# Kernel tuning notes

Hardware: AMD Instinct MI355X
Metric: run time of the kernel (lower is better)

## Reference

```python
import jax, jax.numpy as jnp
import numpy as np

B, H, E = 1024, 2048, 1024

def _xavier(key, shape):
    # torch xavier_normal_ on [1, out, in]: std = sqrt(2/(fan_in+fan_out)) over last two dims
    fan_out, fan_in = shape[-2], shape[-1]
    std = (2.0 / (fan_in + fan_out)) ** 0.5
    return jax.random.normal(key, shape, jnp.float32) * std

def setup_inputs() -> dict:
    key = jax.random.key(0)
    ks = jax.random.split(key, 17)
    inp = {
        'x': jax.random.normal(ks[0], (B, E, 1), jnp.float32),
        'c': jax.random.normal(ks[1], (B, H, 1), jnp.float32),
        'h': jax.random.normal(ks[2], (B, H, 1), jnp.float32),
        'W_xi': _xavier(ks[3], (1, H, E)), 'W_hi': _xavier(ks[4], (1, H, H)), 'B_i': _xavier(ks[5], (1, H, 1)),
        'W_xg': _xavier(ks[6], (1, H, E)), 'W_hg': _xavier(ks[7], (1, H, H)), 'B_g': _xavier(ks[8], (1, H, 1)),
        'W_xf': _xavier(ks[9], (1, H, E)), 'W_hf': _xavier(ks[10], (1, H, H)), 'B_f': _xavier(ks[11], (1, H, 1)),
        'W_xo': _xavier(ks[12], (1, H, E)), 'W_ho': _xavier(ks[13], (1, H, H)), 'B_o': _xavier(ks[14], (1, H, 1)),
        'W_hy': _xavier(ks[15], (1, E, H)), 'B_y': _xavier(ks[16], (1, E, 1)),
    }
    return inp

def reference(x, c, h, W_xi, W_hi, B_i, W_xg, W_hg, B_g, W_xf, W_hf, B_f, W_xo, W_ho, B_o, W_hy, B_y):
    # jnp.matmul broadcasts the leading batch dim: [1,H,E] @ [B,E,1] -> [B,H,1]
    i = jax.nn.sigmoid(jnp.matmul(W_xi, x) + jnp.matmul(W_hi, h) + B_i)
    g = jnp.tanh(jnp.matmul(W_xg, x) + jnp.matmul(W_hg, h) + B_g)
    f = jax.nn.sigmoid(jnp.matmul(W_xf, x) + jnp.matmul(W_hf, h) + B_f)
    c_new = f * c + i * g
    o = jax.nn.sigmoid(jnp.matmul(W_xo, x) + jnp.matmul(W_ho, h) + B_o)
    h_new = o * c_new  # NOTE: source uses o*c (no tanh), faithful to original
    y = jnp.tanh(jnp.matmul(W_hy, h_new) + B_y)
    return (y, c_new, h_new)
```

## Files before the change

kernel.cpp:

```cpp
#include <hip/hip_runtime.h>

#define B_SZ 1024
#define H_SZ 2048
#define E_SZ 1024

typedef float  f32x4 __attribute__((ext_vector_type(4)));
typedef short  s16x8 __attribute__((ext_vector_type(8)));

__device__ __forceinline__ unsigned short f2bf(float f) {
    unsigned u = __float_as_uint(f);
    u = u + 0x7fffu + ((u >> 16) & 1u);
    return (unsigned short)(u >> 16);
}
__device__ __forceinline__ float bf2f(unsigned short s) {
    return __uint_as_float(((unsigned)s) << 16);
}

struct CastArgs {
    const float*    src[11];
    unsigned short* dst[11];
    int             n[11];
};

__global__ __launch_bounds__(256) void cast_kernel(CastArgs a) {
    const int arr = blockIdx.y;
    const int n = a.n[arr];
    const float* __restrict__ s = a.src[arr];
    unsigned short* __restrict__ d = a.dst[arr];
    const int stride = gridDim.x * 256 * 4;
    for (int i = (blockIdx.x * 256 + threadIdx.x) * 4; i < n; i += stride) {
        float4 v = *(const float4*)(s + i);
        ushort4 o;
        o.x = f2bf(v.x); o.y = f2bf(v.y); o.z = f2bf(v.z); o.w = f2bf(v.w);
        *(ushort4*)(d + i) = o;
    }
}

__device__ __forceinline__ void gemm_accum(
    const unsigned short* __restrict__ A,
    const unsigned short* __restrict__ W,
    int ld, int kLen, int m0, int n0,
    unsigned short* lA, unsigned short* lB,
    f32x4 acc[4][4], int t)
{
    const int lane = t & 63;
    const int w    = t >> 6;
    const int wr   = (w >> 1) << 6;
    const int wc   = (w & 1) << 6;
    const int lr   = lane & 15;
    const int kq   = (lane >> 4) << 3;

    const int r0   = t >> 2;
    const int col0 = (t & 3) << 3;

    for (int k0 = 0; k0 < kLen; k0 += 32) {
        const unsigned short* ga0 = A + (size_t)(m0 + r0) * ld + (k0 + col0);
        const unsigned short* ga1 = ga0 + (size_t)64 * ld;
        const unsigned short* gb0 = W + (size_t)(n0 + r0) * ld + (k0 + col0);
        const unsigned short* gb1 = gb0 + (size_t)64 * ld;
        __builtin_amdgcn_global_load_lds(
            (const __attribute__((address_space(1))) unsigned int*)ga0,
            (__attribute__((address_space(3))) unsigned int*)(lA + t * 8), 16, 0, 0);
        __builtin_amdgcn_global_load_lds(
            (const __attribute__((address_space(1))) unsigned int*)ga1,
            (__attribute__((address_space(3))) unsigned int*)(lA + (t + 256) * 8), 16, 0, 0);
        __builtin_amdgcn_global_load_lds(
            (const __attribute__((address_space(1))) unsigned int*)gb0,
            (__attribute__((address_space(3))) unsigned int*)(lB + t * 8), 16, 0, 0);
        __builtin_amdgcn_global_load_lds(
            (const __attribute__((address_space(1))) unsigned int*)gb1,
            (__attribute__((address_space(3))) unsigned int*)(lB + (t + 256) * 8), 16, 0, 0);
        __syncthreads();

        s16x8 af[4], bfr[4];
#pragma unroll
        for (int i = 0; i < 4; ++i)
            af[i] = *(const s16x8*)(lA + (wr + i * 16 + lr) * 32 + kq);
#pragma unroll
        for (int j = 0; j < 4; ++j)
            bfr[j] = *(const s16x8*)(lB + (wc + j * 16 + lr) * 32 + kq);
#pragma unroll
        for (int i = 0; i < 4; ++i)
#pragma unroll
            for (int j = 0; j < 4; ++j)
                acc[i][j] = __builtin_amdgcn_mfma_f32_16x16x32_bf16(
                    af[i], bfr[j], acc[i][j], 0, 0, 0);
        __syncthreads();
    }
}

__global__ __launch_bounds__(256) void gates_kernel(
    const unsigned short* __restrict__ Xb,
    const unsigned short* __restrict__ Hb,
    const unsigned short* __restrict__ Wxb,
    const unsigned short* __restrict__ Whb,
    const float* __restrict__ bi, const float* __restrict__ bg,
    const float* __restrict__ bff, const float* __restrict__ bo,
    unsigned short* __restrict__ Z)
{
    __shared__ unsigned short lA[128 * 32];
    __shared__ unsigned short lB[128 * 32];
    const int t   = threadIdx.x;
    const int b   = blockIdx.x;
    const int xcd = b & 7;
    const int i_  = b >> 3;
    const int nt  = xcd * 8 + (i_ >> 3);
    const int m0  = (i_ & 7) * 128;
    const int q   = nt >> 4;
    const int n0  = (nt & 15) * 128;

    f32x4 acc[4][4] = {};
    gemm_accum(Xb, Wxb + (size_t)q * H_SZ * E_SZ, E_SZ, E_SZ, m0, n0, lA, lB, acc, t);
    gemm_accum(Hb, Whb + (size_t)q * H_SZ * H_SZ, H_SZ, H_SZ, m0, n0, lA, lB, acc, t);

    const float* bias = (q == 0) ? bi : (q == 1) ? bg : (q == 2) ? bff : bo;
    const int lane = t & 63, w = t >> 6;
    const int wr = (w >> 1) << 6, wc = (w & 1) << 6;
    const int lr = lane & 15, rq = (lane >> 4) << 2;
    unsigned short* Zq = Z + (size_t)q * B_SZ * H_SZ;
#pragma unroll
    for (int i = 0; i < 4; ++i) {
#pragma unroll
        for (int j = 0; j < 4; ++j) {
            const int n = n0 + wc + j * 16 + lr;
            const float bv = bias[n];
#pragma unroll
            for (int r = 0; r < 4; ++r) {
                const int m = m0 + wr + i * 16 + rq + r;
                const float v = acc[i][j][r] + bv;
                const float a = (q == 1) ? tanhf(v) : 1.0f / (1.0f + __expf(-v));
                Zq[(size_t)m * H_SZ + n] = f2bf(a);
            }
        }
    }
}

__global__ __launch_bounds__(256) void cell_kernel(
    const unsigned short* __restrict__ Z, const float* __restrict__ c,
    float* __restrict__ c_out, float* __restrict__ h_out,
    unsigned short* __restrict__ HnB)
{
    const size_t BH = (size_t)B_SZ * H_SZ;
    const int idx = (blockIdx.x * 256 + threadIdx.x) * 4;
    ushort4 iu = *(const ushort4*)(Z + idx);
    ushort4 gu = *(const ushort4*)(Z + BH + idx);
    ushort4 fu = *(const ushort4*)(Z + 2 * BH + idx);
    ushort4 ou = *(const ushort4*)(Z + 3 * BH + idx);
    float4 cv = *(const float4*)(c + idx);

    float cn[4], hn[4];
    cn[0] = bf2f(fu.x) * cv.x + bf2f(iu.x) * bf2f(gu.x);
    cn[1] = bf2f(fu.y) * cv.y + bf2f(iu.y) * bf2f(gu.y);
    cn[2] = bf2f(fu.z) * cv.z + bf2f(iu.z) * bf2f(gu.z);
    cn[3] = bf2f(fu.w) * cv.w + bf2f(iu.w) * bf2f(gu.w);
    hn[0] = bf2f(ou.x) * cn[0];
    hn[1] = bf2f(ou.y) * cn[1];
    hn[2] = bf2f(ou.z) * cn[2];
    hn[3] = bf2f(ou.w) * cn[3];

    *(float4*)(c_out + idx) = make_float4(cn[0], cn[1], cn[2], cn[3]);
    *(float4*)(h_out + idx) = make_float4(hn[0], hn[1], hn[2], hn[3]);
    ushort4 hb;
    hb.x = f2bf(hn[0]); hb.y = f2bf(hn[1]); hb.z = f2bf(hn[2]); hb.w = f2bf(hn[3]);
    *(ushort4*)(HnB + idx) = hb;
}

__global__ __launch_bounds__(256) void y_split_kernel(
    const unsigned short* __restrict__ Hn,
    const unsigned short* __restrict__ Wy,
    float* __restrict__ part)
{
    __shared__ unsigned short lA[128 * 32];
    __shared__ unsigned short lB[128 * 32];
    const int t   = threadIdx.x;
    const int b   = blockIdx.x;
    const int xcd = b & 7;
    const int i_  = b >> 3;
    const int ns  = xcd * 4 + (i_ >> 3);
    const int m0  = (i_ & 7) * 128;
    const int n0  = (ns >> 2) * 128;
    const int s   = ns & 3;

    f32x4 acc[4][4] = {};
    gemm_accum(Hn + s * 512, Wy + s * 512, H_SZ, 512, m0, n0, lA, lB, acc, t);

    const int lane = t & 63, w = t >> 6;
    const int wr = (w >> 1) << 6, wc = (w & 1) << 6;
    const int lr = lane & 15, rq = (lane >> 4) << 2;
    float* P = part + (size_t)s * B_SZ * E_SZ;
#pragma unroll
    for (int i = 0; i < 4; ++i) {
#pragma unroll
        for (int j = 0; j < 4; ++j) {
            const int n = n0 + wc + j * 16 + lr;
#pragma unroll
            for (int r = 0; r < 4; ++r) {
                const int m = m0 + wr + i * 16 + rq + r;
                P[(size_t)m * E_SZ + n] = acc[i][j][r];
            }
        }
    }
}

__global__ __launch_bounds__(256) void y_reduce_kernel(
    const float* __restrict__ part, const float* __restrict__ by,
    float* __restrict__ yout)
{
    const size_t BE = (size_t)B_SZ * E_SZ;
    const int idx = (blockIdx.x * 256 + threadIdx.x) * 4;
    float4 a = *(const float4*)(part + idx);
    float4 b2 = *(const float4*)(part + BE + idx);
    float4 c2 = *(const float4*)(part + 2 * BE + idx);
    float4 d2 = *(const float4*)(part + 3 * BE + idx);
    const int col = idx & (E_SZ - 1);
    float4 bv = *(const float4*)(by + col);
    float4 o;
    o.x = tanhf(a.x + b2.x + c2.x + d2.x + bv.x);
    o.y = tanhf(a.y + b2.y + c2.y + d2.y + bv.y);
    o.z = tanhf(a.z + b2.z + c2.z + d2.z + bv.z);
    o.w = tanhf(a.w + b2.w + c2.w + d2.w + bv.w);
    *(float4*)(yout + idx) = o;
}

extern "C" void kernel_launch(void* const* d_in, const int* in_sizes, int n_in,
                              void* d_out, int out_size, void* d_ws, size_t ws_size,
                              hipStream_t stream) {
    const float* x   = (const float*)d_in[0];
    const float* c   = (const float*)d_in[1];
    const float* h   = (const float*)d_in[2];
    const float* Wxi = (const float*)d_in[3];
    const float* Whi = (const float*)d_in[4];
    const float* Bi  = (const float*)d_in[5];
    const float* Wxg = (const float*)d_in[6];
    const float* Whg = (const float*)d_in[7];
    const float* Bg  = (const float*)d_in[8];
    const float* Wxf = (const float*)d_in[9];
    const float* Whf = (const float*)d_in[10];
    const float* Bf  = (const float*)d_in[11];
    const float* Wxo = (const float*)d_in[12];
    const float* Who = (const float*)d_in[13];
    const float* Bo  = (const float*)d_in[14];
    const float* Why = (const float*)d_in[15];
    const float* By  = (const float*)d_in[16];

    const size_t BE = (size_t)B_SZ * E_SZ, BH = (size_t)B_SZ * H_SZ;
    const size_t HE = (size_t)H_SZ * E_SZ, HH = (size_t)H_SZ * H_SZ;
    const size_t EH = (size_t)E_SZ * H_SZ;

    unsigned short* ws   = (unsigned short*)d_ws;
    unsigned short* Xb   = ws;
    unsigned short* Hb   = Xb + BE;
    unsigned short* Wxb  = Hb + BH;
    unsigned short* Whb  = Wxb + 4 * HE;
    unsigned short* Whyb = Whb + 4 * HH;
    unsigned short* Z    = Whyb + EH;
    unsigned short* HnB  = Z + 4 * BH;

    CastArgs ca;
    ca.src[0]  = x;   ca.dst[0]  = Xb;           ca.n[0]  = (int)BE;
    ca.src[1]  = h;   ca.dst[1]  = Hb;           ca.n[1]  = (int)BH;
    ca.src[2]  = Wxi; ca.dst[2]  = Wxb;          ca.n[2]  = (int)HE;
    ca.src[3]  = Wxg; ca.dst[3]  = Wxb + HE;     ca.n[3]  = (int)HE;
    ca.src[4]  = Wxf; ca.dst[4]  = Wxb + 2 * HE; ca.n[4]  = (int)HE;
    ca.src[5]  = Wxo; ca.dst[5]  = Wxb + 3 * HE; ca.n[5]  = (int)HE;
    ca.src[6]  = Whi; ca.dst[6]  = Whb;          ca.n[6]  = (int)HH;
    ca.src[7]  = Whg; ca.dst[7]  = Whb + HH;     ca.n[7]  = (int)HH;
    ca.src[8]  = Whf; ca.dst[8]  = Whb + 2 * HH; ca.n[8]  = (int)HH;
    ca.src[9]  = Who; ca.dst[9]  = Whb + 3 * HH; ca.n[9]  = (int)HH;
    ca.src[10] = Why; ca.dst[10] = Whyb;         ca.n[10] = (int)EH;

    hipLaunchKernelGGL(cast_kernel, dim3(1024, 11), dim3(256), 0, stream, ca);
    hipLaunchKernelGGL(gates_kernel, dim3(512), dim3(256), 0, stream,
                       Xb, Hb, Wxb, Whb, Bi, Bg, Bf, Bo, Z);

    float* y_out = (float*)d_out;
    float* c_out = y_out + BE;
    float* h_out = c_out + BH;
    hipLaunchKernelGGL(cell_kernel, dim3((unsigned)(BH / 1024)), dim3(256), 0, stream,
                       Z, c, c_out, h_out, HnB);

    float* part = (float*)Z;
    hipLaunchKernelGGL(y_split_kernel, dim3(256), dim3(256), 0, stream,
                       HnB, Whyb, part);
    hipLaunchKernelGGL(y_reduce_kernel, dim3((unsigned)(BE / 1024)), dim3(256), 0, stream,
                       part, By, y_out);
}
```

Measured before the change: 281.2 us.

## Split gates GEMM K dimension in two and fuse activations into combine kernel

The gates GEMM now runs as 1024 workgroups instead of 512. It splits the K=3072 reduction into two halves (x plus the first 512 of h, then the remaining 1536 of h), and each half writes a raw bf16 partial sum. The bias, activations and cell update move into a combine kernel that sums the two partials. The aim is better CU occupancy on a 256-CU device, since 512 workgroups underfill it. The cost is twice the partial-sum traffic, and partials rounded to bf16 before the nonlinearity lose some accuracy.

```diff
diff --git a/kernel.cpp b/kernel.cpp
--- a/kernel.cpp
+++ b/kernel.cpp
@@ -14,6 +14,9 @@
 }
 __device__ __forceinline__ float bf2f(unsigned short s) {
     return __uint_as_float(((unsigned)s) << 16);
+}
+__device__ __forceinline__ float sigm(float v) {
+    return 1.0f / (1.0f + __expf(-v));
 }
 
 struct CastArgs {
@@ -94,9 +97,7 @@
     const unsigned short* __restrict__ Hb,
     const unsigned short* __restrict__ Wxb,
     const unsigned short* __restrict__ Whb,
-    const float* __restrict__ bi, const float* __restrict__ bg,
-    const float* __restrict__ bff, const float* __restrict__ bo,
-    unsigned short* __restrict__ Z)
+    unsigned short* __restrict__ part)
 {
     __shared__ unsigned short lA[128 * 32];
     __shared__ unsigned short lB[128 * 32];
@@ -104,60 +105,84 @@
     const int b   = blockIdx.x;
     const int xcd = b & 7;
     const int i_  = b >> 3;
-    const int nt  = xcd * 8 + (i_ >> 3);
-    const int m0  = (i_ & 7) * 128;
+    const int nt  = xcd * 8 + (i_ >> 4);
+    const int rem = i_ & 15;
+    const int m0  = (rem & 7) * 128;
+    const int s   = rem >> 3;
     const int q   = nt >> 4;
     const int n0  = (nt & 15) * 128;
 
     f32x4 acc[4][4] = {};
-    gemm_accum(Xb, Wxb + (size_t)q * H_SZ * E_SZ, E_SZ, E_SZ, m0, n0, lA, lB, acc, t);
-    gemm_accum(Hb, Whb + (size_t)q * H_SZ * H_SZ, H_SZ, H_SZ, m0, n0, lA, lB, acc, t);
-
-    const float* bias = (q == 0) ? bi : (q == 1) ? bg : (q == 2) ? bff : bo;
+    if (s == 0) {
+        gemm_accum(Xb, Wxb + (size_t)q * H_SZ * E_SZ, E_SZ, E_SZ, m0, n0, lA, lB, acc, t);
+        gemm_accum(Hb, Whb + (size_t)q * H_SZ * H_SZ, H_SZ, 512, m0, n0, lA, lB, acc, t);
+    } else {
+        gemm_accum(Hb + 512, Whb + (size_t)q * H_SZ * H_SZ + 512, H_SZ, 1536,
+                   m0, n0, lA, lB, acc, t);
+    }
+
     const int lane = t & 63, w = t >> 6;
     const int wr = (w >> 1) << 6, wc = (w & 1) << 6;
     const int lr = lane & 15, rq = (lane >> 4) << 2;
-    unsigned short* Zq = Z + (size_t)q * B_SZ * H_SZ;
+    unsigned short* P = part + (size_t)(s * 4 + q) * B_SZ * H_SZ;
 #pragma unroll
     for (int i = 0; i < 4; ++i) {
 #pragma unroll
         for (int j = 0; j < 4; ++j) {
             const int n = n0 + wc + j * 16 + lr;
-            const float bv = bias[n];
 #pragma unroll
             for (int r = 0; r < 4; ++r) {
                 const int m = m0 + wr + i * 16 + rq + r;
-                const float v = acc[i][j][r] + bv;
-                const float a = (q == 1) ? tanhf(v) : 1.0f / (1.0f + __expf(-v));
-                Zq[(size_t)m * H_SZ + n] = f2bf(a);
+                P[(size_t)m * H_SZ + n] = f2bf(acc[i][j][r]);
             }
         }
     }
 }
 
-__global__ __launch_bounds__(256) void cell_kernel(
-    const unsigned short* __restrict__ Z, const float* __restrict__ c,
+__global__ __launch_bounds__(256) void combine_kernel(
+    const unsigned short* __restrict__ part,
+    const float* __restrict__ bi, const float* __restrict__ bg,
+    const float* __restrict__ bff, const float* __restrict__ bo,
+    const float* __restrict__ c,
     float* __restrict__ c_out, float* __restrict__ h_out,
     unsigned short* __restrict__ HnB)
 {
     const size_t BH = (size_t)B_SZ * H_SZ;
     const int idx = (blockIdx.x * 256 + threadIdx.x) * 4;
-    ushort4 iu = *(const ushort4*)(Z + idx);
-    ushort4 gu = *(const ushort4*)(Z + BH + idx);
-    ushort4 fu = *(const ushort4*)(Z + 2 * BH + idx);
-    ushort4 ou = *(const ushort4*)(Z + 3 * BH + idx);
-    float4 cv = *(const float4*)(c + idx);
+    const int col = idx & (H_SZ - 1);
+
+    float v[4][4];
+#pragma unroll
+    for (int q = 0; q < 4; ++q) {
+        ushort4 p0 = *(const ushort4*)(part + (size_t)q * BH + idx);
+        ushort4 p1 = *(const ushort4*)(part + (size_t)(4 + q) * BH + idx);
+        v[q][0] = bf2f(p0.x) + bf2f(p1.x);
+        v[q][1] = bf2f(p0.y) + bf2f(p1.y);
+        v[q][2] = bf2f(p0.z) + bf2f(p1.z);
+        v[q][3] = bf2f(p0.w) + bf2f(p1.w);
+    }
+    float4 bvi = *(const float4*)(bi + col);
+    float4 bvg = *(const float4*)(bg + col);
+    float4 bvf = *(const float4*)(bff + col);
+    float4 bvo = *(const float4*)(bo + col);
+    float4 cv  = *(const float4*)(c + idx);
+
+    const float bi_[4] = {bvi.x, bvi.y, bvi.z, bvi.w};
+    const float bg_[4] = {bvg.x, bvg.y, bvg.z, bvg.w};
+    const float bf_[4] = {bvf.x, bvf.y, bvf.z, bvf.w};
+    const float bo_[4] = {bvo.x, bvo.y, bvo.z, bvo.w};
+    const float c_[4]  = {cv.x, cv.y, cv.z, cv.w};
 
     float cn[4], hn[4];
-    cn[0] = bf2f(fu.x) * cv.x + bf2f(iu.x) * bf2f(gu.x);
-    cn[1] = bf2f(fu.y) * cv.y + bf2f(iu.y) * bf2f(gu.y);
-    cn[2] = bf2f(fu.z) * cv.z + bf2f(iu.z) * bf2f(gu.z);
-    cn[3] = bf2f(fu.w) * cv.w + bf2f(iu.w) * bf2f(gu.w);
-    hn[0] = bf2f(ou.x) * cn[0];
-    hn[1] = bf2f(ou.y) * cn[1];
-    hn[2] = bf2f(ou.z) * cn[2];
-    hn[3] = bf2f(ou.w) * cn[3];
-
+#pragma unroll
+    for (int e = 0; e < 4; ++e) {
+        const float iv = sigm(v[0][e] + bi_[e]);
+        const float gv = tanhf(v[1][e] + bg_[e]);
+        const float fv = sigm(v[2][e] + bf_[e]);
+        const float ov = sigm(v[3][e] + bo_[e]);
+        cn[e] = fv * c_[e] + iv * gv;
+        hn[e] = ov * cn[e];
+    }
     *(float4*)(c_out + idx) = make_float4(cn[0], cn[1], cn[2], cn[3]);
     *(float4*)(h_out + idx) = make_float4(hn[0], hn[1], hn[2], hn[3]);
     ushort4 hb;
@@ -253,8 +278,8 @@
     unsigned short* Wxb  = Hb + BH;
     unsigned short* Whb  = Wxb + 4 * HE;
     unsigned short* Whyb = Whb + 4 * HH;
-    unsigned short* Z    = Whyb + EH;
-    unsigned short* HnB  = Z + 4 * BH;
+    unsigned short* Gp   = Whyb + EH;
+    unsigned short* HnB  = Gp + 8 * BH;
 
     CastArgs ca;
     ca.src[0]  = x;   ca.dst[0]  = Xb;           ca.n[0]  = (int)BE;
@@ -270,18 +295,18 @@
     ca.src[10] = Why; ca.dst[10] = Whyb;         ca.n[10] = (int)EH;
 
     hipLaunchKernelGGL(cast_kernel, dim3(1024, 11), dim3(256), 0, stream, ca);
-    hipLaunchKernelGGL(gates_kernel, dim3(512), dim3(256), 0, stream,
-                       Xb, Hb, Wxb, Whb, Bi, Bg, Bf, Bo, Z);
+    hipLaunchKernelGGL(gates_kernel, dim3(1024), dim3(256), 0, stream,
+                       Xb, Hb, Wxb, Whb, Gp);
 
     float* y_out = (float*)d_out;
     float* c_out = y_out + BE;
     float* h_out = c_out + BH;
-    hipLaunchKernelGGL(cell_kernel, dim3((unsigned)(BH / 1024)), dim3(256), 0, stream,
-                       Z, c, c_out, h_out, HnB);
-
-    float* part = (float*)Z;
+    hipLaunchKernelGGL(combine_kernel, dim3((unsigned)(BH / 1024)), dim3(256), 0, stream,
+                       Gp, Bi, Bg, Bf, Bo, c, c_out, h_out, HnB);
+
+    float* ypart = (float*)Gp;
     hipLaunchKernelGGL(y_split_kernel, dim3(256), dim3(256), 0, stream,
-                       HnB, Whyb, part);
+                       HnB, Whyb, ypart);
     hipLaunchKernelGGL(y_reduce_kernel, dim3((unsigned)(BE / 1024)), dim3(256), 0, stream,
-                       part, By, y_out);
-}
+                       ypart, By, y_out);
+}
```

After: 288.7 us. 2.7% more time.

## Double-buffer LDS tiles with async global-to-LDS prefetch in GEMM kernels

Applied to the files above, without the earlier changes.

Replaces the shared gemm_accum helper with inline double-buffered loops in both the gates and y_split kernels. Each loop keeps two K-steps of global_load_lds in flight and uses explicit vmcnt/lgkmcnt waits and barriers instead of __syncthreads around every tile. The goal is to hide global memory latency behind MFMA work. In exchange, LDS use per block doubles, which may lower occupancy, and the hand-set waitcnt encodings must be correct for the target.

```diff
diff --git a/kernel.cpp b/kernel.cpp
--- a/kernel.cpp
+++ b/kernel.cpp
@@ -15,6 +15,19 @@
 __device__ __forceinline__ float bf2f(unsigned short s) {
     return __uint_as_float(((unsigned)s) << 16);
 }
+__device__ __forceinline__ float sigm(float v) {
+    return 1.0f / (1.0f + __expf(-v));
+}
+
+__device__ __forceinline__ void gll(const unsigned short* g, unsigned short* l) {
+    __builtin_amdgcn_global_load_lds(
+        (const __attribute__((address_space(1))) unsigned int*)g,
+        (__attribute__((address_space(3))) unsigned int*)l, 16, 0, 0);
+}
+
+#define WC_VM4   0x0F74
+#define WC_VM0   0x0F70
+#define WC_LGKM0 0xC07F
 
 struct CastArgs {
     const float*    src[11];
@@ -36,59 +49,6 @@
     }
 }
 
-__device__ __forceinline__ void gemm_accum(
-    const unsigned short* __restrict__ A,
-    const unsigned short* __restrict__ W,
-    int ld, int kLen, int m0, int n0,
-    unsigned short* lA, unsigned short* lB,
-    f32x4 acc[4][4], int t)
-{
-    const int lane = t & 63;
-    const int w    = t >> 6;
-    const int wr   = (w >> 1) << 6;
-    const int wc   = (w & 1) << 6;
-    const int lr   = lane & 15;
-    const int kq   = (lane >> 4) << 3;
-
-    const int r0   = t >> 2;
-    const int col0 = (t & 3) << 3;
-
-    for (int k0 = 0; k0 < kLen; k0 += 32) {
-        const unsigned short* ga0 = A + (size_t)(m0 + r0) * ld + (k0 + col0);
-        const unsigned short* ga1 = ga0 + (size_t)64 * ld;
-        const unsigned short* gb0 = W + (size_t)(n0 + r0) * ld + (k0 + col0);
-        const unsigned short* gb1 = gb0 + (size_t)64 * ld;
-        __builtin_amdgcn_global_load_lds(
-            (const __attribute__((address_space(1))) unsigned int*)ga0,
-            (__attribute__((address_space(3))) unsigned int*)(lA + t * 8), 16, 0, 0);
-        __builtin_amdgcn_global_load_lds(
-            (const __attribute__((address_space(1))) unsigned int*)ga1,
-            (__attribute__((address_space(3))) unsigned int*)(lA + (t + 256) * 8), 16, 0, 0);
-        __builtin_amdgcn_global_load_lds(
-            (const __attribute__((address_space(1))) unsigned int*)gb0,
-            (__attribute__((address_space(3))) unsigned int*)(lB + t * 8), 16, 0, 0);
-        __builtin_amdgcn_global_load_lds(
-            (const __attribute__((address_space(1))) unsigned int*)gb1,
-            (__attribute__((address_space(3))) unsigned int*)(lB + (t + 256) * 8), 16, 0, 0);
-        __syncthreads();
-
-        s16x8 af[4], bfr[4];
-#pragma unroll
-        for (int i = 0; i < 4; ++i)
-            af[i] = *(const s16x8*)(lA + (wr + i * 16 + lr) * 32 + kq);
-#pragma unroll
-        for (int j = 0; j < 4; ++j)
-            bfr[j] = *(const s16x8*)(lB + (wc + j * 16 + lr) * 32 + kq);
-#pragma unroll
-        for (int i = 0; i < 4; ++i)
-#pragma unroll
-            for (int j = 0; j < 4; ++j)
-                acc[i][j] = __builtin_amdgcn_mfma_f32_16x16x32_bf16(
-                    af[i], bfr[j], acc[i][j], 0, 0, 0);
-        __syncthreads();
-    }
-}
-
 __global__ __launch_bounds__(256) void gates_kernel(
     const unsigned short* __restrict__ Xb,
     const unsigned short* __restrict__ Hb,
@@ -98,8 +58,8 @@
     const float* __restrict__ bff, const float* __restrict__ bo,
     unsigned short* __restrict__ Z)
 {
-    __shared__ unsigned short lA[128 * 32];
-    __shared__ unsigned short lB[128 * 32];
+    __shared__ unsigned short lA[2 * 4096];
+    __shared__ unsigned short lB[2 * 4096];
     const int t   = threadIdx.x;
     const int b   = blockIdx.x;
     const int xcd = b & 7;
@@ -109,14 +69,70 @@
     const int q   = nt >> 4;
     const int n0  = (nt & 15) * 128;
 
-    f32x4 acc[4][4] = {};
-    gemm_accum(Xb, Wxb + (size_t)q * H_SZ * E_SZ, E_SZ, E_SZ, m0, n0, lA, lB, acc, t);
-    gemm_accum(Hb, Whb + (size_t)q * H_SZ * H_SZ, H_SZ, H_SZ, m0, n0, lA, lB, acc, t);
-
-    const float* bias = (q == 0) ? bi : (q == 1) ? bg : (q == 2) ? bff : bo;
+    const int r0   = t >> 2;
+    const int col0 = (t & 3) << 3;
+
+    const unsigned short* Wx = Wxb + (size_t)q * H_SZ * E_SZ;
+    const unsigned short* Wh = Whb + (size_t)q * H_SZ * H_SZ;
+    const unsigned short* baseAx = Xb + (size_t)(m0 + r0) * E_SZ + col0;
+    const unsigned short* baseBx = Wx + (size_t)(n0 + r0) * E_SZ + col0;
+    const unsigned short* baseAh = Hb + (size_t)(m0 + r0) * H_SZ + col0;
+    const unsigned short* baseBh = Wh + (size_t)(n0 + r0) * H_SZ + col0;
+
     const int lane = t & 63, w = t >> 6;
     const int wr = (w >> 1) << 6, wc = (w & 1) << 6;
-    const int lr = lane & 15, rq = (lane >> 4) << 2;
+    const int lr = lane & 15, kq = (lane >> 4) << 3;
+
+#define ISSUE(s, buf) do {                                                  \
+        const unsigned short *a0_, *b0_; size_t st_;                        \
+        if ((s) < 32) { a0_ = baseAx + (s) * 32; b0_ = baseBx + (s) * 32;   \
+                        st_ = (size_t)64 * E_SZ; }                          \
+        else          { a0_ = baseAh + ((s) - 32) * 32;                     \
+                        b0_ = baseBh + ((s) - 32) * 32;                     \
+                        st_ = (size_t)64 * H_SZ; }                          \
+        unsigned short* la_ = lA + (buf) * 4096;                            \
+        unsigned short* lb_ = lB + (buf) * 4096;                            \
+        gll(a0_,       la_ + t * 8);                                        \
+        gll(a0_ + st_, la_ + (t + 256) * 8);                                \
+        gll(b0_,       lb_ + t * 8);                                        \
+        gll(b0_ + st_, lb_ + (t + 256) * 8);                                \
+    } while (0)
+
+    f32x4 acc[4][4] = {};
+    ISSUE(0, 0);
+    ISSUE(1, 1);
+
+    for (int k = 0; k < 96; ++k) {
+        const int cur = k & 1;
+        if (k < 95) __builtin_amdgcn_s_waitcnt(WC_VM4);
+        else        __builtin_amdgcn_s_waitcnt(WC_VM0);
+        __builtin_amdgcn_s_barrier();
+
+        const unsigned short* la = lA + cur * 4096;
+        const unsigned short* lb = lB + cur * 4096;
+        s16x8 af[4], bfr[4];
+#pragma unroll
+        for (int i = 0; i < 4; ++i)
+            af[i] = *(const s16x8*)(la + (wr + i * 16 + lr) * 32 + kq);
+#pragma unroll
+        for (int j = 0; j < 4; ++j)
+            bfr[j] = *(const s16x8*)(lb + (wc + j * 16 + lr) * 32 + kq);
+
+        __builtin_amdgcn_s_waitcnt(WC_LGKM0);
+        __builtin_amdgcn_s_barrier();
+        if (k + 2 < 96) ISSUE(k + 2, cur);
+
+#pragma unroll
+        for (int i = 0; i < 4; ++i)
+#pragma unroll
+            for (int j = 0; j < 4; ++j)
+                acc[i][j] = __builtin_amdgcn_mfma_f32_16x16x32_bf16(
+                    af[i], bfr[j], acc[i][j], 0, 0, 0);
+    }
+#undef ISSUE
+
+    const float* bias = (q == 0) ? bi : (q == 1) ? bg : (q == 2) ? bff : bo;
+    const int rq = (lane >> 4) << 2;
     unsigned short* Zq = Z + (size_t)q * B_SZ * H_SZ;
 #pragma unroll
     for (int i = 0; i < 4; ++i) {
@@ -128,7 +144,7 @@
             for (int r = 0; r < 4; ++r) {
                 const int m = m0 + wr + i * 16 + rq + r;
                 const float v = acc[i][j][r] + bv;
-                const float a = (q == 1) ? tanhf(v) : 1.0f / (1.0f + __expf(-v));
+                const float a = (q == 1) ? tanhf(v) : sigm(v);
                 Zq[(size_t)m * H_SZ + n] = f2bf(a);
             }
         }
@@ -170,8 +186,8 @@
     const unsigned short* __restrict__ Wy,
     float* __restrict__ part)
 {
-    __shared__ unsigned short lA[128 * 32];
-    __shared__ unsigned short lB[128 * 32];
+    __shared__ unsigned short lA[2 * 4096];
+    __shared__ unsigned short lB[2 * 4096];
     const int t   = threadIdx.x;
     const int b   = blockIdx.x;
     const int xcd = b & 7;
@@ -181,12 +197,57 @@
     const int n0  = (ns >> 2) * 128;
     const int s   = ns & 3;
 
-    f32x4 acc[4][4] = {};
-    gemm_accum(Hn + s * 512, Wy + s * 512, H_SZ, 512, m0, n0, lA, lB, acc, t);
+    const int r0   = t >> 2;
+    const int col0 = (t & 3) << 3;
+    const unsigned short* baseA = Hn + (size_t)(m0 + r0) * H_SZ + s * 512 + col0;
+    const unsigned short* baseB = Wy + (size_t)(n0 + r0) * H_SZ + s * 512 + col0;
+    const size_t st = (size_t)64 * H_SZ;
 
     const int lane = t & 63, w = t >> 6;
     const int wr = (w >> 1) << 6, wc = (w & 1) << 6;
-    const int lr = lane & 15, rq = (lane >> 4) << 2;
+    const int lr = lane & 15, kq = (lane >> 4) << 3;
+
+#define ISSUE(sp, buf) do {                                                 \
+        const unsigned short* a0_ = baseA + (sp) * 32;                      \
+        const unsigned short* b0_ = baseB + (sp) * 32;                      \
+        unsigned short* la_ = lA + (buf) * 4096;                            \
+        unsigned short* lb_ = lB + (buf) * 4096;                            \
+        gll(a0_,      la_ + t * 8);                                         \
+        gll(a0_ + st, la_ + (t + 256) * 8);                                 \
+        gll(b0_,      lb_ + t * 8);                                         \
+        gll(b0_ + st, lb_ + (t + 256) * 8);                                 \
+    } while (0)
+
+    f32x4 acc[4][4] = {};
+    ISSUE(0, 0);
+    ISSUE(1, 1);
+    for (int k = 0; k < 16; ++k) {
+        const int cur = k & 1;
+        if (k < 15) __builtin_amdgcn_s_waitcnt(WC_VM4);
+        else        __builtin_amdgcn_s_waitcnt(WC_VM0);
+        __builtin_amdgcn_s_barrier();
+        const unsigned short* la = lA + cur * 4096;
+        const unsigned short* lb = lB + cur * 4096;
+        s16x8 af[4], bfr[4];
+#pragma unroll
+        for (int i = 0; i < 4; ++i)
+            af[i] = *(const s16x8*)(la + (wr + i * 16 + lr) * 32 + kq);
+#pragma unroll
+        for (int j = 0; j < 4; ++j)
+            bfr[j] = *(const s16x8*)(lb + (wc + j * 16 + lr) * 32 + kq);
+        __builtin_amdgcn_s_waitcnt(WC_LGKM0);
+        __builtin_amdgcn_s_barrier();
+        if (k + 2 < 16) ISSUE(k + 2, cur);
+#pragma unroll
+        for (int i = 0; i < 4; ++i)
+#pragma unroll
+            for (int j = 0; j < 4; ++j)
+                acc[i][j] = __builtin_amdgcn_mfma_f32_16x16x32_bf16(
+                    af[i], bfr[j], acc[i][j], 0, 0, 0);
+    }
+#undef ISSUE
+
+    const int rq = (lane >> 4) << 2;
     float* P = part + (size_t)s * B_SZ * E_SZ;
 #pragma unroll
     for (int i = 0; i < 4; ++i) {
@@ -279,9 +340,9 @@
     hipLaunchKernelGGL(cell_kernel, dim3((unsigned)(BH / 1024)), dim3(256), 0, stream,
                        Z, c, c_out, h_out, HnB);
 
-    float* part = (float*)Z;
+    float* ypart = (float*)Z;
     hipLaunchKernelGGL(y_split_kernel, dim3(256), dim3(256), 0, stream,
-                       HnB, Whyb, part);
+                       HnB, Whyb, ypart);
     hipLaunchKernelGGL(y_reduce_kernel, dim3((unsigned)(BE / 1024)), dim3(256), 0, stream,
-                       part, By, y_out);
-}
+                       ypart, By, y_out);
+}
```

Result: slower. 287.1 us (+2.1%).
